# Kernel optimization log

Hardware: AMD Instinct MI355X
Metric: run time of the kernel (lower is better)

The kernel has to match this reference:

```python
import jax, jax.numpy as jnp
import numpy as np
from itertools import combinations

TEMPERATURE = 0.1
EPS = 1e-8  # matches torch F.cosine_similarity eps

B, D = 4096, 512

def setup_inputs() -> dict:
    key = jax.random.key(0)
    k0, k1, k2 = jax.random.split(key, 3)
    return {
        "z0": jax.random.normal(k0, (B, D), dtype=jnp.float32),
        "z1": jax.random.normal(k1, (B, D), dtype=jnp.float32),
        "z2": jax.random.normal(k2, (B, D), dtype=jnp.float32),
    }

def _normalize(z):
    # cosine_similarity(a,b) == dot(a_hat, b_hat) with norms clamped at eps
    n = jnp.sqrt(jnp.sum(z * z, axis=-1, keepdims=True))
    return z / jnp.maximum(n, EPS)

def _ce(logits):
    # cross entropy with labels = arange(B): -log_softmax(logits)[i, i], mean over rows
    lse = jax.nn.logsumexp(logits, axis=1)          # [B]
    diag = jnp.diagonal(logits)                     # [B]
    return jnp.mean(lse - diag)

def reference(z0, z1, z2):
    latents = [z0, z1, z2]
    normed = [_normalize(z) for z in latents]
    pairs = list(combinations(range(len(latents)), 2))
    total = jnp.asarray(0.0, dtype=z0.dtype)
    for i, j in pairs:
        sim = jnp.einsum("bd,cd->bc", normed[i], normed[j]) / TEMPERATURE  # [B,B]
        total = total + ( _ce(sim) + _ce(sim.T) ) / 2
    return total / max(len(pairs), 1)
```

## Files before the change

### kernel.cpp

```cpp
#include <hip/hip_runtime.h>
#include <hip/hip_bf16.h>

#define NB 4096
#define ND 512

typedef int i32x4 __attribute__((ext_vector_type(4)));
typedef int i32x8 __attribute__((ext_vector_type(8)));
typedef float f32x4 __attribute__((ext_vector_type(4)));

#define AS1 __attribute__((address_space(1)))
#define AS3 __attribute__((address_space(3)))

__device__ __forceinline__ float fexp2(float x) {
    float r;
    asm("v_exp_f32 %0, %1" : "=v"(r) : "v"(x));
    return r;
}

__device__ __forceinline__ unsigned int f2e4m3(float x) {
    float a = fabsf(x);
    unsigned s = (__float_as_uint(x) >> 24) & 0x80u;
    if (a < 0.015625f) {
        int q = __float2int_rn(a * 512.0f);
        return s | (unsigned)q;
    }
    unsigned u = __float_as_uint(a);
    u += 0x7FFFFu + ((u >> 20) & 1u);
    unsigned e8 = (u >> 23) - 120u;
    unsigned m = (u >> 20) & 7u;
    return s | (e8 << 3) | m;
}

__global__ __launch_bounds__(256) void nrm_kernel(
    const float* __restrict__ z0, const float* __restrict__ z1,
    const float* __restrict__ z2, unsigned char* __restrict__ nrm8,
    float* __restrict__ rowsum, float* __restrict__ colsum)
{
    const int w = threadIdx.x >> 6, lane = threadIdx.x & 63;
    const int row = blockIdx.x * 4 + w;
    const int p = blockIdx.y;
    if (lane == 0) {
        rowsum[p * NB + row] = 0.f;
        colsum[p * NB + row] = 0.f;
    }
    const float* z = (p == 0) ? z0 : (p == 1) ? z1 : z2;
    const float4* zr = (const float4*)(z + (size_t)row * ND);
    const float4 a = zr[lane * 2], b = zr[lane * 2 + 1];
    float ss = a.x * a.x + a.y * a.y + a.z * a.z + a.w * a.w
             + b.x * b.x + b.y * b.y + b.z * b.z + b.w * b.w;
    #pragma unroll
    for (int m = 32; m >= 1; m >>= 1) ss += __shfl_xor(ss, m);
    const float inv = 1.0f / fmaxf(sqrtf(ss), 1e-8f);
    uint2 o;
    o.x = f2e4m3(a.x * inv) | (f2e4m3(a.y * inv) << 8)
        | (f2e4m3(a.z * inv) << 16) | (f2e4m3(a.w * inv) << 24);
    o.y = f2e4m3(b.x * inv) | (f2e4m3(b.y * inv) << 8)
        | (f2e4m3(b.z * inv) << 16) | (f2e4m3(b.w * inv) << 24);
    *(uint2*)(nrm8 + ((size_t)p * NB + row) * ND + lane * 8) = o;
}

__global__ __launch_bounds__(256, 2) void pair_gemm_kernel(
    const unsigned char* __restrict__ nrm8,
    float* __restrict__ rowsum, float* __restrict__ colsum,
    float* __restrict__ diag)
{
    const int bid = blockIdx.x;
    const int bxc = bid & 7;
    const int r = bid >> 3;
    const int p = r >> 5;
    const int by = r & 31;
    const int ia = (p == 2) ? 1 : 0;
    const int ib = (p == 0) ? 1 : 2;

    const char* Ag = (const char*)nrm8 + ((size_t)ia * NB + (size_t)by * 128) * ND;
    const char* Bg = (const char*)nrm8 + ((size_t)ib * NB + (size_t)bxc * 512) * ND;

    __shared__ char lds[65536];

    const int tid = threadIdx.x;
    const int lane = tid & 63;
    const int w = tid >> 6;
    const int wr = w >> 1, wc = w & 1;
    const int lr = lane & 15, lg = lane >> 4;

    int srcOff[4];
    #pragma unroll
    for (int q = 0; q < 4; ++q) {
        const int c = q * 256 + tid;
        const int rr = c >> 3;
        srcOff[q] = rr * ND + (((c & 7) ^ (rr & 7)) * 16);
    }

    const int s0 = ((2 * lg) ^ (lr & 7)) * 16;
    const int s1 = ((2 * lg + 1) ^ (lr & 7)) * 16;
    int arow[4], brow[4];
    #pragma unroll
    for (int m = 0; m < 4; ++m) {
        arow[m] = (wr * 64 + m * 16 + lr) * 128;
        brow[m] = (wc * 64 + m * 16 + lr) * 128;
    }

    f32x4 acc[4][4] = {};
    float rs[4][4];
    #pragma unroll
    for (int m = 0; m < 4; ++m)
        #pragma unroll
        for (int j = 0; j < 4; ++j) rs[m][j] = 0.f;

    #define STAGE(gsrc, dstbase) do {                                               \
        _Pragma("unroll")                                                           \
        for (int q = 0; q < 4; ++q)                                                 \
            __builtin_amdgcn_global_load_lds(                                       \
                (const AS1 void*)((gsrc) + srcOff[q]),                              \
                (AS3 void*)(lds + (dstbase) + q * 4096 + tid * 16), 16, 0, 0);      \
    } while (0)

    #define LDF(dst, base) do {                                                     \
        i32x4 lo_ = *(const i32x4*)((base) + s0);                                   \
        i32x4 hi_ = *(const i32x4*)((base) + s1);                                   \
        dst = __builtin_shufflevector(lo_, hi_, 0, 1, 2, 3, 4, 5, 6, 7);            \
    } while (0)

    #define SC 0x7F7F7F7F
    constexpr float C10 = 14.42695040888963f;

    STAGE(Ag, 0);
    STAGE(Bg, 32768);
    STAGE(Ag + 128, 16384);
    STAGE(Bg + 128, 32768 + 16384);
    asm volatile("s_waitcnt vmcnt(8)" ::: "memory");
    __builtin_amdgcn_s_barrier();

    #pragma unroll 1
    for (int s = 0; s < 16; ++s) {
        const int bxl = s >> 2, k = s & 3;
        const int pb = s & 1;

        const char* ab = lds + pb * 16384;
        const char* bb = lds + 32768 + pb * 16384;
        i32x8 af[4], bf[4];
        #pragma unroll
        for (int m = 0; m < 4; ++m) LDF(af[m], ab + arow[m]);
        #pragma unroll
        for (int n = 0; n < 4; ++n) LDF(bf[n], bb + brow[n]);

        if (s < 14) {
            asm volatile("s_waitcnt lgkmcnt(0)" ::: "memory");
            __builtin_amdgcn_s_barrier();
            const int s2 = s + 2;
            STAGE(Ag + (s2 & 3) * 128, pb * 16384);
            STAGE(Bg + (size_t)(s2 >> 2) * 128 * ND + (s2 & 3) * 128,
                  32768 + pb * 16384);
        }

        __builtin_amdgcn_s_setprio(1);
        #pragma unroll
        for (int m = 0; m < 4; ++m)
            #pragma unroll
            for (int n = 0; n < 4; ++n)
                acc[m][n] = __builtin_amdgcn_mfma_scale_f32_16x16x128_f8f6f4(
                    af[m], bf[n], acc[m][n], 0, 0, 0, SC, 0, SC);
        __builtin_amdgcn_s_setprio(0);

        if (k == 3) {
            const int bxg = bxc * 4 + bxl;
            if (by == bxg && wr == wc) {
                #pragma unroll
                for (int m = 0; m < 4; ++m)
                    #pragma unroll
                    for (int j = 0; j < 4; ++j)
                        if (lr == lg * 4 + j)
                            diag[p * NB + by * 128 + wr * 64 + m * 16 + lr] = acc[m][m][j];
            }
            float cs[4] = {0.f, 0.f, 0.f, 0.f};
            #pragma unroll
            for (int m = 0; m < 4; ++m)
                #pragma unroll
                for (int n = 0; n < 4; ++n)
                    #pragma unroll
                    for (int j = 0; j < 4; ++j) {
                        float e = fexp2(fmaf(acc[m][n][j], C10, -C10));
                        rs[m][j] += e;
                        cs[n] += e;
                    }
            #pragma unroll
            for (int n = 0; n < 4; ++n) {
                float v = cs[n];
                v += __shfl_xor(v, 16);
                v += __shfl_xor(v, 32);
                if (lg == 0)
                    atomicAdd(&colsum[p * NB + bxg * 128 + wc * 64 + n * 16 + lr], v);
            }
            #pragma unroll
            for (int m = 0; m < 4; ++m)
                #pragma unroll
                for (int n = 0; n < 4; ++n)
                    acc[m][n] = (f32x4){0.f, 0.f, 0.f, 0.f};
        }

        if (s < 14) {
            if (k == 3) asm volatile("s_waitcnt vmcnt(12)" ::: "memory");
            else        asm volatile("s_waitcnt vmcnt(8)" ::: "memory");
            __builtin_amdgcn_s_barrier();
        } else if (s == 14) {
            asm volatile("s_waitcnt vmcnt(0)" ::: "memory");
            __builtin_amdgcn_s_barrier();
        }
    }
    #undef STAGE
    #undef LDF

    #pragma unroll
    for (int m = 0; m < 4; ++m)
        #pragma unroll
        for (int j = 0; j < 4; ++j) {
            float v = rs[m][j];
            v += __shfl_xor(v, 1);
            v += __shfl_xor(v, 2);
            v += __shfl_xor(v, 4);
            v += __shfl_xor(v, 8);
            if (lr == 0)
                atomicAdd(&rowsum[p * NB + by * 128 + wr * 64 + m * 16 + lg * 4 + j], v);
        }
}

__global__ __launch_bounds__(256) void finalize_kernel(
    const float* __restrict__ rowsum, const float* __restrict__ colsum,
    const float* __restrict__ diag, float* __restrict__ out)
{
    const int i = blockIdx.x * 256 + threadIdx.x;
    float s = 0.5f * (logf(rowsum[i]) + logf(colsum[i])) + 10.0f - 10.0f * diag[i];
    #pragma unroll
    for (int m = 32; m >= 1; m >>= 1) s += __shfl_xor(s, m);
    __shared__ float sw[4];
    if ((threadIdx.x & 63) == 0) sw[threadIdx.x >> 6] = s;
    __syncthreads();
    if (threadIdx.x == 0)
        atomicAdd(out, (sw[0] + sw[1] + sw[2] + sw[3]) * (1.0f / (3.0f * NB)));
}

extern "C" void kernel_launch(void* const* d_in, const int* in_sizes, int n_in,
                              void* d_out, int out_size, void* d_ws, size_t ws_size,
                              hipStream_t stream) {
    const float* z0 = (const float*)d_in[0];
    const float* z1 = (const float*)d_in[1];
    const float* z2 = (const float*)d_in[2];
    float* out = (float*)d_out;

    char* ws = (char*)d_ws;
    unsigned char* nrm8 = (unsigned char*)ws;
    const size_t nrm_bytes = (size_t)3 * NB * ND;
    float* rowsum = (float*)(ws + nrm_bytes);
    float* colsum = rowsum + 3 * NB;
    float* diag = colsum + 3 * NB;

    hipMemsetAsync(out, 0, sizeof(float), stream);
    nrm_kernel<<<dim3(NB / 4, 3), 256, 0, stream>>>(z0, z1, z2, nrm8, rowsum, colsum);
    pair_gemm_kernel<<<768, 256, 0, stream>>>(nrm8, rowsum, colsum, diag);
    finalize_kernel<<<48, 256, 0, stream>>>(rowsum, colsum, diag, out);
}
```

Measured before the change: 61.99 us.

## Remap pair GEMM to 512 persistent blocks each processing six tiles

The pair GEMM grid goes from 768 blocks of four 128x128 tiles to 512 blocks of six tiles. A block's tiles may now span different row blocks and pairs. Each tile's A/B addresses are recomputed per unit, and row sums are flushed with atomics whenever the row block changes. The aim is to remove the partial second wave, since 512 blocks at two per CU should fill the device in one wave. The cost is extra address arithmetic, occasional mid-loop flushes with a deeper vmcnt wait, and more rowsum atomics.

```diff
diff --git a/kernel.cpp b/kernel.cpp
--- a/kernel.cpp
+++ b/kernel.cpp
@@ -59,21 +59,27 @@
     *(uint2*)(nrm8 + ((size_t)p * NB + row) * ND + lane * 8) = o;
 }
 
+struct UnitInfo { const char* Ag; const char* Bg; int p, by, bx; };
+__device__ __forceinline__ UnitInfo unit_info(const unsigned char* nrm8, int U) {
+    UnitInfo t;
+    t.p = U >> 10;
+    const int rem = U & 1023;
+    t.by = rem >> 5;
+    t.bx = rem & 31;
+    const int ia = (t.p == 2) ? 1 : 0;
+    const int ib = (t.p == 0) ? 1 : 2;
+    t.Ag = (const char*)nrm8 + ((size_t)ia * NB + (size_t)t.by * 128) * ND;
+    t.Bg = (const char*)nrm8 + ((size_t)ib * NB + (size_t)t.bx * 128) * ND;
+    return t;
+}
+
 __global__ __launch_bounds__(256, 2) void pair_gemm_kernel(
     const unsigned char* __restrict__ nrm8,
     float* __restrict__ rowsum, float* __restrict__ colsum,
     float* __restrict__ diag)
 {
     const int bid = blockIdx.x;
-    const int bxc = bid & 7;
-    const int r = bid >> 3;
-    const int p = r >> 5;
-    const int by = r & 31;
-    const int ia = (p == 2) ? 1 : 0;
-    const int ib = (p == 0) ? 1 : 2;
-
-    const char* Ag = (const char*)nrm8 + ((size_t)ia * NB + (size_t)by * 128) * ND;
-    const char* Bg = (const char*)nrm8 + ((size_t)ib * NB + (size_t)bxc * 512) * ND;
+    const int base = (bid & 7) * 384 + (bid >> 3) * 6;
 
     __shared__ char lds[65536];
 
@@ -115,26 +121,46 @@
                 (AS3 void*)(lds + (dstbase) + q * 4096 + tid * 16), 16, 0, 0);      \
     } while (0)
 
-    #define LDF(dst, base) do {                                                     \
-        i32x4 lo_ = *(const i32x4*)((base) + s0);                                   \
-        i32x4 hi_ = *(const i32x4*)((base) + s1);                                   \
+    #define LDF(dst, base_) do {                                                    \
+        i32x4 lo_ = *(const i32x4*)((base_) + s0);                                  \
+        i32x4 hi_ = *(const i32x4*)((base_) + s1);                                  \
         dst = __builtin_shufflevector(lo_, hi_, 0, 1, 2, 3, 4, 5, 6, 7);            \
     } while (0)
 
+    #define FLUSH_RS(P, BY) do {                                                    \
+        _Pragma("unroll")                                                           \
+        for (int m = 0; m < 4; ++m)                                                 \
+            _Pragma("unroll")                                                       \
+            for (int j = 0; j < 4; ++j) {                                           \
+                float v = rs[m][j];                                                 \
+                v += __shfl_xor(v, 1);                                              \
+                v += __shfl_xor(v, 2);                                              \
+                v += __shfl_xor(v, 4);                                              \
+                v += __shfl_xor(v, 8);                                              \
+                if (lr == 0)                                                        \
+                    atomicAdd(&rowsum[(P) * NB + (BY) * 128 + wr * 64 + m * 16 + lg * 4 + j], v); \
+                rs[m][j] = 0.f;                                                     \
+            }                                                                       \
+    } while (0)
+
     #define SC 0x7F7F7F7F
     constexpr float C10 = 14.42695040888963f;
 
-    STAGE(Ag, 0);
-    STAGE(Bg, 32768);
-    STAGE(Ag + 128, 16384);
-    STAGE(Bg + 128, 32768 + 16384);
+    {
+        UnitInfo u0 = unit_info(nrm8, base);
+        STAGE(u0.Ag, 0);
+        STAGE(u0.Bg, 32768);
+        STAGE(u0.Ag + 128, 16384);
+        STAGE(u0.Bg + 128, 32768 + 16384);
+    }
     asm volatile("s_waitcnt vmcnt(8)" ::: "memory");
     __builtin_amdgcn_s_barrier();
 
     #pragma unroll 1
-    for (int s = 0; s < 16; ++s) {
-        const int bxl = s >> 2, k = s & 3;
+    for (int s = 0; s < 24; ++s) {
+        const int u = s >> 2, k = s & 3;
         const int pb = s & 1;
+        const UnitInfo cur = unit_info(nrm8, base + u);
 
         const char* ab = lds + pb * 16384;
         const char* bb = lds + 32768 + pb * 16384;
@@ -144,13 +170,13 @@
         #pragma unroll
         for (int n = 0; n < 4; ++n) LDF(bf[n], bb + brow[n]);
 
-        if (s < 14) {
+        if (s < 22) {
             asm volatile("s_waitcnt lgkmcnt(0)" ::: "memory");
             __builtin_amdgcn_s_barrier();
             const int s2 = s + 2;
-            STAGE(Ag + (s2 & 3) * 128, pb * 16384);
-            STAGE(Bg + (size_t)(s2 >> 2) * 128 * ND + (s2 & 3) * 128,
-                  32768 + pb * 16384);
+            const UnitInfo nx = unit_info(nrm8, base + (s2 >> 2));
+            STAGE(nx.Ag + (s2 & 3) * 128, pb * 16384);
+            STAGE(nx.Bg + (s2 & 3) * 128, 32768 + pb * 16384);
         }
 
         __builtin_amdgcn_s_setprio(1);
@@ -162,15 +188,15 @@
                     af[m], bf[n], acc[m][n], 0, 0, 0, SC, 0, SC);
         __builtin_amdgcn_s_setprio(0);
 
+        bool flush = false;
         if (k == 3) {
-            const int bxg = bxc * 4 + bxl;
-            if (by == bxg && wr == wc) {
+            if (cur.by == cur.bx && wr == wc) {
                 #pragma unroll
                 for (int m = 0; m < 4; ++m)
                     #pragma unroll
                     for (int j = 0; j < 4; ++j)
                         if (lr == lg * 4 + j)
-                            diag[p * NB + by * 128 + wr * 64 + m * 16 + lr] = acc[m][m][j];
+                            diag[cur.p * NB + cur.by * 128 + wr * 64 + m * 16 + lr] = acc[m][m][j];
             }
             float cs[4] = {0.f, 0.f, 0.f, 0.f};
             #pragma unroll
@@ -189,8 +215,10 @@
                 v += __shfl_xor(v, 16);
                 v += __shfl_xor(v, 32);
                 if (lg == 0)
-                    atomicAdd(&colsum[p * NB + bxg * 128 + wc * 64 + n * 16 + lr], v);
+                    atomicAdd(&colsum[cur.p * NB + cur.bx * 128 + wc * 64 + n * 16 + lr], v);
             }
+            flush = (u < 5) && (((base + u + 1) >> 5) != ((base + u) >> 5));
+            if (flush) FLUSH_RS(cur.p, cur.by);
             #pragma unroll
             for (int m = 0; m < 4; ++m)
                 #pragma unroll
@@ -198,11 +226,12 @@
                     acc[m][n] = (f32x4){0.f, 0.f, 0.f, 0.f};
         }
 
-        if (s < 14) {
-            if (k == 3) asm volatile("s_waitcnt vmcnt(12)" ::: "memory");
-            else        asm volatile("s_waitcnt vmcnt(8)" ::: "memory");
+        if (s < 22) {
+            if (flush)       asm volatile("s_waitcnt vmcnt(28)" ::: "memory");
+            else if (k == 3) asm volatile("s_waitcnt vmcnt(12)" ::: "memory");
+            else             asm volatile("s_waitcnt vmcnt(8)" ::: "memory");
             __builtin_amdgcn_s_barrier();
-        } else if (s == 14) {
+        } else if (s == 22) {
             asm volatile("s_waitcnt vmcnt(0)" ::: "memory");
             __builtin_amdgcn_s_barrier();
         }
@@ -210,18 +239,11 @@
     #undef STAGE
     #undef LDF
 
-    #pragma unroll
-    for (int m = 0; m < 4; ++m)
-        #pragma unroll
-        for (int j = 0; j < 4; ++j) {
-            float v = rs[m][j];
-            v += __shfl_xor(v, 1);
-            v += __shfl_xor(v, 2);
-            v += __shfl_xor(v, 4);
-            v += __shfl_xor(v, 8);
-            if (lr == 0)
-                atomicAdd(&rowsum[p * NB + by * 128 + wr * 64 + m * 16 + lg * 4 + j], v);
-        }
+    {
+        const UnitInfo last = unit_info(nrm8, base + 5);
+        FLUSH_RS(last.p, last.by);
+    }
+    #undef FLUSH_RS
 }
 
 __global__ __launch_bounds__(256) void finalize_kernel(
@@ -256,6 +278,6 @@
 
     hipMemsetAsync(out, 0, sizeof(float), stream);
     nrm_kernel<<<dim3(NB / 4, 3), 256, 0, stream>>>(z0, z1, z2, nrm8, rowsum, colsum);
-    pair_gemm_kernel<<<768, 256, 0, stream>>>(nrm8, rowsum, colsum, diag);
+    pair_gemm_kernel<<<512, 256, 0, stream>>>(nrm8, rowsum, colsum, diag);
     finalize_kernel<<<48, 256, 0, stream>>>(rowsum, colsum, diag, out);
 }
```

Result: faster. 60.06 us (-3.1%).

## Single-buffer A tile to cut LDS and allow three blocks per CU

Applied to the files above, without the earlier changes.

The A operand now uses one LDS slot instead of a double buffer, so LDS per block drops from 64KB to 48KB and launch bounds go from 2 to 3 blocks per CU. The vmcnt waits and the prefetch schedule are adjusted to match. Block indices are remapped so each XCD covers a contiguous range of tiles, and each block handles four adjacent column tiles. This targets low occupancy and poor cache locality, but the next A chunk is now loaded only one step ahead, which exposes more load latency and could add register pressure under the tighter bound.

```diff
diff --git a/kernel.cpp b/kernel.cpp
--- a/kernel.cpp
+++ b/kernel.cpp
@@ -59,23 +59,24 @@
     *(uint2*)(nrm8 + ((size_t)p * NB + row) * ND + lane * 8) = o;
 }
 
-__global__ __launch_bounds__(256, 2) void pair_gemm_kernel(
+__global__ __launch_bounds__(256, 3) void pair_gemm_kernel(
     const unsigned char* __restrict__ nrm8,
     float* __restrict__ rowsum, float* __restrict__ colsum,
     float* __restrict__ diag)
 {
     const int bid = blockIdx.x;
-    const int bxc = bid & 7;
-    const int r = bid >> 3;
-    const int p = r >> 5;
-    const int by = r & 31;
+    const int base = (bid & 7) * 384 + (bid >> 3) * 4;
+    const int p = base >> 10;
+    const int rem = base & 1023;
+    const int by = rem >> 5;
+    const int bx0 = rem & 31;
     const int ia = (p == 2) ? 1 : 0;
     const int ib = (p == 0) ? 1 : 2;
 
     const char* Ag = (const char*)nrm8 + ((size_t)ia * NB + (size_t)by * 128) * ND;
-    const char* Bg = (const char*)nrm8 + ((size_t)ib * NB + (size_t)bxc * 512) * ND;
-
-    __shared__ char lds[65536];
+    const char* Bg = (const char*)nrm8 + ((size_t)ib * NB + (size_t)bx0 * 128) * ND;
+
+    __shared__ char lds[49152];
 
     const int tid = threadIdx.x;
     const int lane = tid & 63;
@@ -115,9 +116,9 @@
                 (AS3 void*)(lds + (dstbase) + q * 4096 + tid * 16), 16, 0, 0);      \
     } while (0)
 
-    #define LDF(dst, base) do {                                                     \
-        i32x4 lo_ = *(const i32x4*)((base) + s0);                                   \
-        i32x4 hi_ = *(const i32x4*)((base) + s1);                                   \
+    #define LDF(dst, base_) do {                                                    \
+        i32x4 lo_ = *(const i32x4*)((base_) + s0);                                  \
+        i32x4 hi_ = *(const i32x4*)((base_) + s1);                                  \
         dst = __builtin_shufflevector(lo_, hi_, 0, 1, 2, 3, 4, 5, 6, 7);            \
     } while (0)
 
@@ -125,32 +126,32 @@
     constexpr float C10 = 14.42695040888963f;
 
     STAGE(Ag, 0);
-    STAGE(Bg, 32768);
-    STAGE(Ag + 128, 16384);
-    STAGE(Bg + 128, 32768 + 16384);
-    asm volatile("s_waitcnt vmcnt(8)" ::: "memory");
+    STAGE(Bg, 16384);
+    STAGE(Bg + 128, 32768);
+    asm volatile("s_waitcnt vmcnt(4)" ::: "memory");
     __builtin_amdgcn_s_barrier();
 
     #pragma unroll 1
     for (int s = 0; s < 16; ++s) {
-        const int bxl = s >> 2, k = s & 3;
+        const int u = s >> 2, k = s & 3;
         const int pb = s & 1;
 
-        const char* ab = lds + pb * 16384;
-        const char* bb = lds + 32768 + pb * 16384;
+        const char* bb = lds + 16384 + pb * 16384;
         i32x8 af[4], bf[4];
         #pragma unroll
-        for (int m = 0; m < 4; ++m) LDF(af[m], ab + arow[m]);
+        for (int m = 0; m < 4; ++m) LDF(af[m], lds + arow[m]);
         #pragma unroll
         for (int n = 0; n < 4; ++n) LDF(bf[n], bb + brow[n]);
 
-        if (s < 14) {
+        if (s < 15) {
             asm volatile("s_waitcnt lgkmcnt(0)" ::: "memory");
             __builtin_amdgcn_s_barrier();
-            const int s2 = s + 2;
-            STAGE(Ag + (s2 & 3) * 128, pb * 16384);
-            STAGE(Bg + (size_t)(s2 >> 2) * 128 * ND + (s2 & 3) * 128,
-                  32768 + pb * 16384);
+            STAGE(Ag + ((s + 1) & 3) * 128, 0);
+            if (s < 14) {
+                const int s2 = s + 2;
+                STAGE(Bg + (size_t)(s2 >> 2) * 65536 + (s2 & 3) * 128,
+                      16384 + pb * 16384);
+            }
         }
 
         __builtin_amdgcn_s_setprio(1);
@@ -163,7 +164,7 @@
         __builtin_amdgcn_s_setprio(0);
 
         if (k == 3) {
-            const int bxg = bxc * 4 + bxl;
+            const int bxg = bx0 + u;
             if (by == bxg && wr == wc) {
                 #pragma unroll
                 for (int m = 0; m < 4; ++m)
@@ -199,8 +200,8 @@
         }
 
         if (s < 14) {
-            if (k == 3) asm volatile("s_waitcnt vmcnt(12)" ::: "memory");
-            else        asm volatile("s_waitcnt vmcnt(8)" ::: "memory");
+            if (k == 3) asm volatile("s_waitcnt vmcnt(8)" ::: "memory");
+            else        asm volatile("s_waitcnt vmcnt(4)" ::: "memory");
             __builtin_amdgcn_s_barrier();
         } else if (s == 14) {
             asm volatile("s_waitcnt vmcnt(0)" ::: "memory");
```

New measurement: 57.76 us. -6.8%, faster.
